# Kernel tuning notes

Measured on AMD Instinct MI355X. Metric: run time of the kernel, lower is better.

Reference implementation:

```python
import jax, jax.numpy as jnp
import numpy as np

N_NODES, IN_DIM, HID, LAT, N_EDGES = 50000, 3000, 512, 30, 800000
NEG_SLOPE = 0.2


def setup_inputs() -> dict:
    key = jax.random.key(0)
    ks = jax.random.split(key, 6)
    x = jax.random.normal(ks[0], (N_NODES, IN_DIM), dtype=jnp.float32)
    edge_index = jax.random.randint(ks[1], (2, N_EDGES), 0, N_NODES, dtype=jnp.int64)
    # xavier-normal-ish scales
    W1 = jax.random.normal(ks[2], (IN_DIM, HID), dtype=jnp.float32) * 0.02
    W2 = jax.random.normal(ks[3], (HID, LAT), dtype=jnp.float32) * 0.06
    att_src = jax.random.normal(ks[4], (HID,), dtype=jnp.float32) * 0.1
    att_dst = jax.random.normal(ks[5], (HID,), dtype=jnp.float32) * 0.1
    return {"x": x, "edge_index": edge_index, "W1": W1, "W2": W2,
            "att_src": att_src, "att_dst": att_dst}


def _segment_softmax(e, seg, num_segments):
    # numerically stable softmax over variable-degree dst neighborhoods
    m = jax.ops.segment_max(e, seg, num_segments=num_segments)
    m = jnp.where(jnp.isfinite(m), m, 0.0)  # empty segments -> 0, harmless
    p = jnp.exp(e - m[seg])
    s = jax.ops.segment_sum(p, seg, num_segments=num_segments)
    return p / (s[seg] + 1e-16)


def reference(x, edge_index, W1, W2, att_src, att_dst):
    N = x.shape[0]
    src, dst = edge_index[0], edge_index[1]  # messages flow src(j) -> dst(i)

    # ---- conv1: full GAT layer (heads=1, no self-loops, no bias) ----
    h1 = x @ W1                                   # [N, 512]
    a_src = h1 @ att_src                          # [N]
    a_dst = h1 @ att_dst                          # [N]
    e = jax.nn.leaky_relu(a_src[src] + a_dst[dst], NEG_SLOPE)  # [E]
    alpha = _segment_softmax(e, dst, N)           # [E] (also tied attn for conv3)
    agg1 = jax.ops.segment_sum(h1[src] * alpha[:, None], dst, num_segments=N)
    x1 = jax.nn.elu(agg1)                         # [N, 512]

    # ---- conv2: attention=False -> plain linear projection ----
    x2 = x1 @ W2                                  # [N, 30] (latent embedding)

    # ---- conv3: tied weights (W2^T) + tied attention from conv1 ----
    h3 = x2 @ W2.T                                # [N, 512]
    agg3 = jax.ops.segment_sum(h3[src] * alpha[:, None], dst, num_segments=N)
    x3 = jax.nn.elu(agg3)

    # ---- conv4: attention=False, tied weights (W1^T) ----
    x4 = x3 @ W1.T                                # [N, in_channels]
    return (x2, x4)
```

## Files before the change

### kernel.cpp

```cpp
#include <hip/hip_runtime.h>

#define N_NODES 50000
#define IN_DIM  3000
#define HID     512
#define LAT     30
#define N_EDGES 800000
#define M_PAD   50048
#define M_PAD2  50176
#define K1_PAD  3008
#define N4_PAD  3072

typedef __bf16 bf16;
typedef unsigned int uint;
typedef __attribute__((ext_vector_type(4))) float f32x4;
typedef __attribute__((ext_vector_type(8))) bf16 bf16x8;

__device__ __forceinline__ float bf2f(bf16 b){ return (float)b; }

__device__ __forceinline__ void gl16(const void* g, void* l){
  __builtin_amdgcn_global_load_lds(
      (const __attribute__((address_space(1))) void*)g,
      (__attribute__((address_space(3))) void*)l, 16, 0, 0);
}

__device__ __forceinline__ int xcd_swz(int orig, int nwg){
  int q = nwg >> 3, r = nwg & 7;
  int xcd = orig & 7, lid = orig >> 3;
  return (xcd < r ? xcd*(q+1) : r*(q+1) + (xcd-r)*q) + lid;
}

__global__ void k_w1t(const float* __restrict__ W1, bf16* __restrict__ W1T){
  int k = blockIdx.x*256 + threadIdx.x;
  int n = blockIdx.y;
  if (k >= K1_PAD) return;
  float v = (k < IN_DIM) ? W1[(long)k*HID + n] : 0.f;
  int kt = k >> 6, c = (k >> 3) & 7, off = k & 7;
  int p = c ^ (n & 7);
  W1T[(long)n*K1_PAD + kt*64 + p*8 + off] = (bf16)v;
}
__global__ void k_w1p(const float* __restrict__ W1, bf16* __restrict__ W1P){
  int k = blockIdx.x*256 + threadIdx.x;
  int n = blockIdx.y;
  if (k >= HID) return;
  float v = (n < IN_DIM) ? W1[(long)n*HID + k] : 0.f;
  int kt = k >> 6, c = (k >> 3) & 7, off = k & 7;
  int p = c ^ (n & 7);
  W1P[(long)n*HID + kt*64 + p*8 + off] = (bf16)v;
}
__global__ void k_w2t(const float* __restrict__ W2, bf16* __restrict__ W2T){
  int k = blockIdx.x*256 + threadIdx.x;
  int n = blockIdx.y;
  if (k >= HID) return;
  float v = (n < LAT) ? W2[(long)k*LAT + n] : 0.f;
  W2T[(long)n*HID + k] = (bf16)v;
}
__global__ void k_w2p(const float* __restrict__ W2, bf16* __restrict__ W2P){
  int t = blockIdx.x*256 + threadIdx.x;
  if (t >= HID*32) return;
  int n = t >> 5, k = t & 31;
  W2P[t] = (bf16)((k < LAT) ? W2[(long)n*LAT + k] : 0.f);
}

__global__ __launch_bounds__(256) void k_cvt(const float* __restrict__ x, bf16* __restrict__ xb){
  int chunk = blockIdx.x*256 + threadIdx.x;
  int row = blockIdx.y;
  if (chunk >= K1_PAD/8) return;
  int c8 = chunk*8;
  bf16x8 o;
  if (row < N_NODES && c8 + 8 <= IN_DIM){
    float4 v0 = *(const float4*)(x + (long)row*IN_DIM + c8);
    float4 v1 = *(const float4*)(x + (long)row*IN_DIM + c8 + 4);
    o[0]=(bf16)v0.x; o[1]=(bf16)v0.y; o[2]=(bf16)v0.z; o[3]=(bf16)v0.w;
    o[4]=(bf16)v1.x; o[5]=(bf16)v1.y; o[6]=(bf16)v1.z; o[7]=(bf16)v1.w;
  } else {
    #pragma unroll
    for (int j=0;j<8;j++){
      int c = c8 + j;
      float v = (row < N_NODES && c < IN_DIM) ? x[(long)row*IN_DIM + c] : 0.f;
      o[j] = (bf16)v;
    }
  }
  *(bf16x8*)(xb + (long)row*K1_PAD + c8) = o;
}

template<bool C_F32>
__global__ __launch_bounds__(512) void gemm8(
    const bf16* __restrict__ Agp, const bf16* __restrict__ Bgp, void* __restrict__ Cp,
    int lda, int ldb, int NT, int Mvalid, int Nvalid, int ldc, int NBX)
{
  __shared__ bf16 Af[2][256*64];
  __shared__ bf16 Bf[2][128*64];
  const int tid  = threadIdx.x;
  const int lane = tid & 63;
  const int w    = tid >> 6;
  const int wm   = (w >> 1) * 64;
  const int wn   = (w & 1) * 64;
  const int wgid = xcd_swz(blockIdx.x, gridDim.x);
  const int col0 = (wgid % NBX) * 128, row0 = (wgid / NBX) * 256;

  const int g   = lane >> 4;
  const int rl  = lane & 15;
  const int rx7 = rl & 7;

  f32x4 acc[4][4];
  #pragma unroll
  for (int mi=0;mi<4;mi++)
    #pragma unroll
    for (int ni=0;ni<4;ni++)
      acc[mi][ni] = (f32x4){0.f,0.f,0.f,0.f};

  bf16x8 a[4][2], B0[4][2], B1[4][2];

#define STAGE8(SLOT, T) do{                                                     \
    const long kb_ = (long)(T)*64;                                              \
    char* la_ = (char*)&Af[SLOT][0] + tid*16;                                   \
    _Pragma("unroll")                                                           \
    for (int i_=0;i_<4;i_++){                                                   \
      int row_ = i_*64 + (tid>>3);                                              \
      gl16(Agp + (long)(row0+row_)*lda + kb_ + (((tid&7)^(row_&7))<<3),         \
           la_ + i_*8192);                                                      \
    }                                                                           \
    char* lb_ = (char*)&Bf[SLOT][0] + tid*16;                                   \
    _Pragma("unroll")                                                           \
    for (int i_=0;i_<2;i_++){                                                   \
      int row_ = i_*64 + (tid>>3);                                              \
      gl16(Bgp + (long)(col0+row_)*ldb + kb_ + ((tid&7)<<3),                    \
           lb_ + i_*8192);                                                      \
    }                                                                           \
  }while(0)

#define RD_A(S, Q, KS) (*(const bf16x8*)((const char*)&Af[S][0] + \
    (wm + (Q)*16 + rl)*128 + ((((KS)*4 + g) ^ rx7)<<4)))
#define RD_B(S, NQ, KS) (*(const bf16x8*)((const char*)&Bf[S][0] + \
    (wn + (NQ)*16 + rl)*128 + ((((KS)*4 + g) ^ rx7)<<4)))

#define PHASE8(Q, BC, BN, SLOTN, DORD) do{                                      \
    __builtin_amdgcn_s_setprio(1);                                              \
    _Pragma("unroll")                                                           \
    for (int ni=0;ni<4;ni++)                                                    \
      acc[Q][ni] = __builtin_amdgcn_mfma_f32_16x16x32_bf16(a[Q][0], BC[ni][0], acc[Q][ni],0,0,0); \
    _Pragma("unroll")                                                           \
    for (int ni=0;ni<4;ni++)                                                    \
      acc[Q][ni] = __builtin_amdgcn_mfma_f32_16x16x32_bf16(a[Q][1], BC[ni][1], acc[Q][ni],0,0,0); \
    __builtin_amdgcn_s_setprio(0);                                              \
    if (DORD){                                                                  \
      a[Q][0]  = RD_A(SLOTN, Q, 0);  a[Q][1]  = RD_A(SLOTN, Q, 1);              \
      BN[Q][0] = RD_B(SLOTN, Q, 0);  BN[Q][1] = RD_B(SLOTN, Q, 1);              \
    }                                                                           \
  }while(0)

#define ITER8(T, SLOT, SLOTN, BC, BN) do{                                       \
    asm volatile("s_waitcnt vmcnt(0) lgkmcnt(0)" ::: "memory");                 \
    __builtin_amdgcn_s_barrier();                                               \
    __builtin_amdgcn_sched_barrier(0);                                          \
    if ((T)+2 < NT) STAGE8(SLOT, (T)+2);                                        \
    const bool dord_ = ((T)+1 < NT);                                            \
    PHASE8(0, BC, BN, SLOTN, dord_);                                            \
    PHASE8(1, BC, BN, SLOTN, dord_);                                            \
    PHASE8(2, BC, BN, SLOTN, dord_);                                            \
    PHASE8(3, BC, BN, SLOTN, dord_);                                            \
  }while(0)

  STAGE8(0, 0);
  asm volatile("s_waitcnt vmcnt(0)" ::: "memory");
  __builtin_amdgcn_s_barrier();
  if (NT > 1) STAGE8(1, 1);
  #pragma unroll
  for (int q=0;q<4;q++){
    a[q][0]  = RD_A(0, q, 0);  a[q][1]  = RD_A(0, q, 1);
    B0[q][0] = RD_B(0, q, 0);  B0[q][1] = RD_B(0, q, 1);
  }

  int t = 0;
  for (; t+1 < NT; t += 2){
    ITER8(t,   0, 1, B0, B1);
    ITER8(t+1, 1, 0, B1, B0);
  }
  if (t < NT) ITER8(t, 0, 1, B0, B1);

#undef ITER8
#undef PHASE8
#undef RD_A
#undef RD_B
#undef STAGE8

  const int crb  = (lane >> 4) * 4;
  const int ccol = lane & 15;
  #pragma unroll
  for (int mi=0;mi<4;mi++){
    #pragma unroll
    for (int v=0;v<4;v++){
      int r = row0 + wm + mi*16 + crb + v;
      if (r >= Mvalid) continue;
      #pragma unroll
      for (int ni=0;ni<4;ni++){
        int c = col0 + wn + ni*16 + ccol;
        if (c >= Nvalid) continue;
        float val = acc[mi][ni][v];
        if (C_F32) ((float*)Cp)[(long)r*ldc + c] = val;
        else       ((bf16*)Cp)[(long)r*ldc + c] = (bf16)val;
      }
    }
  }
}

template<bool C_F32, bool ELU>
__global__ __launch_bounds__(256) void gemm_glds(
    const bf16* __restrict__ A, const bf16* __restrict__ B, void* __restrict__ Cp,
    int lda, int ldb, int Ksteps, int Mvalid, int Nvalid, int ldc, int NBX)
{
  __shared__ bf16 Alds[2][128*32];
  __shared__ bf16 Blds[2][128*32];
  const int tid  = threadIdx.x;
  const int lane = tid & 63;
  const int w    = tid >> 6;
  const int wm   = (w >> 1) * 64, wn = (w & 1) * 64;
  const int wgid = xcd_swz(blockIdx.x, gridDim.x);
  const int col0 = (wgid % NBX) * 128, row0 = (wgid / NBX) * 128;

  f32x4 acc[4][4];
  #pragma unroll
  for (int mi=0;mi<4;mi++)
    #pragma unroll
    for (int ni=0;ni<4;ni++)
      acc[mi][ni] = (f32x4){0.f,0.f,0.f,0.f};

  const int sr = tid >> 2;
  const int sc = (tid & 3) * 16;
  const char* ga = (const char*)(A + (long)(row0 + sr) * lda) + sc;
  const char* gb = (const char*)(B + (long)(col0 + sr) * ldb) + sc;
  const long astep = (long)64 * lda * 2;
  const long bstep = (long)64 * ldb * 2;

#define STAGE_G(buf, ks) do{                                            \
    const long ko_ = (long)(ks) * 64;                                   \
    char* la_ = (char*)&Alds[buf][0] + sr*64 + sc;                      \
    char* lb_ = (char*)&Blds[buf][0] + sr*64 + sc;                      \
    gl16(ga + ko_,         la_);                                        \
    gl16(ga + ko_ + astep, la_ + 64*64);                                \
    gl16(gb + ko_,         lb_);                                        \
    gl16(gb + ko_ + bstep, lb_ + 64*64);                                \
  }while(0)

  STAGE_G(0, 0);

  for (int ks = 0; ks < Ksteps; ks++){
    const int cur = ks & 1;
    if (ks + 1 < Ksteps){
      STAGE_G(cur^1, ks+1);
      asm volatile("s_waitcnt vmcnt(4)" ::: "memory");
    } else {
      asm volatile("s_waitcnt vmcnt(0)" ::: "memory");
    }
    __builtin_amdgcn_s_barrier();

    const bf16* Ac = &Alds[cur][0];
    const bf16* Bc = &Blds[cur][0];
    bf16x8 af[4], bfr[4];
    #pragma unroll
    for (int mi=0;mi<4;mi++)
      af[mi] = *(const bf16x8*)&Ac[(wm + mi*16 + (lane & 15))*32 + (lane>>4)*8];
    #pragma unroll
    for (int ni=0;ni<4;ni++)
      bfr[ni] = *(const bf16x8*)&Bc[(wn + ni*16 + (lane & 15))*32 + (lane>>4)*8];
    #pragma unroll
    for (int mi=0;mi<4;mi++)
      #pragma unroll
      for (int ni=0;ni<4;ni++)
        acc[mi][ni] = __builtin_amdgcn_mfma_f32_16x16x32_bf16(af[mi], bfr[ni], acc[mi][ni], 0, 0, 0);

    __builtin_amdgcn_s_barrier();
  }
#undef STAGE_G

  const int crb  = (lane >> 4) * 4;
  const int ccol = lane & 15;
  #pragma unroll
  for (int mi=0;mi<4;mi++){
    #pragma unroll
    for (int v=0;v<4;v++){
      int r = row0 + wm + mi*16 + crb + v;
      if (r >= Mvalid) continue;
      #pragma unroll
      for (int ni=0;ni<4;ni++){
        int c = col0 + wn + ni*16 + ccol;
        if (c >= Nvalid) continue;
        float val = acc[mi][ni][v];
        if (ELU) val = (val > 0.f) ? val : expm1f(val);
        if (C_F32) ((float*)Cp)[(long)r*ldc + c] = val;
        else       ((bf16*)Cp)[(long)r*ldc + c] = (bf16)val;
      }
    }
  }
}

__global__ void k_attdots(const bf16* __restrict__ h1, const float* __restrict__ att_s,
                          const float* __restrict__ att_d, float* __restrict__ a_src,
                          float* __restrict__ a_dst){
  int gid = blockIdx.x * blockDim.x + threadIdx.x;
  int row = gid >> 6, lane = gid & 63;
  if (row >= N_NODES) return;
  bf16x8 hv = *(const bf16x8*)(h1 + (long)row*HID + lane*8);
  float s1 = 0.f, s2 = 0.f;
  #pragma unroll
  for (int j=0;j<8;j++){
    float h = bf2f(hv[j]);
    s1 = fmaf(h, att_s[lane*8+j], s1);
    s2 = fmaf(h, att_d[lane*8+j], s2);
  }
  #pragma unroll
  for (int o=32;o>0;o>>=1){ s1 += __shfl_down(s1,o); s2 += __shfl_down(s2,o); }
  if (lane == 0){ a_src[row] = s1; a_dst[row] = s2; }
}

__global__ void k_deg(const int* __restrict__ ei, int* __restrict__ deg){
  int e = blockIdx.x*256 + threadIdx.x;
  if (e >= N_EDGES) return;
  atomicAdd(&deg[ei[N_EDGES + e]], 1);
}

__global__ void k_scan(const int* __restrict__ deg, int* __restrict__ off, int* __restrict__ cur){
  const int n = M_PAD, T = 1024;
  int t = threadIdx.x;
  const int per = (n + T - 1) / T;
  int s0 = t*per, s1 = min(n, s0+per);
  int sum = 0;
  for (int i=s0;i<s1;i++) sum += deg[i];
  __shared__ int sd[1024];
  sd[t] = sum; __syncthreads();
  for (int o=1;o<T;o<<=1){
    int x = (t>=o) ? sd[t-o] : 0;
    __syncthreads();
    sd[t] += x;
    __syncthreads();
  }
  int run = sd[t] - sum;
  for (int i=s0;i<s1;i++){
    off[i] = run; cur[i] = run;
    run += deg[i];
  }
  if (s0 < n && s1 == n) off[n] = run;
}

__global__ void k_fill(const int* __restrict__ ei, int* __restrict__ cur,
                       int* __restrict__ csr_src, const float* __restrict__ a_s,
                       const float* __restrict__ a_d, float* __restrict__ p_e){
  int e = blockIdx.x*256 + threadIdx.x;
  if (e >= N_EDGES) return;
  int s = ei[e];
  int d = ei[N_EDGES + e];
  int pos = atomicAdd(&cur[d], 1);
  csr_src[pos] = s;
  float v = a_s[s] + a_d[d];
  v = (v > 0.f) ? v : 0.2f*v;
  p_e[pos] = __expf(v);
}

__global__ __launch_bounds__(256) void k_agg1w(
    const int* __restrict__ off, const int* __restrict__ csr_src,
    const float* __restrict__ p_edge,
    const bf16* __restrict__ h1, bf16* __restrict__ x1,
    float* __restrict__ s_node)
{
  const int i = blockIdx.x*4 + (threadIdx.x >> 6);
  const int lane = threadIdx.x & 63;
  if (i >= N_NODES) return;
  const int start = off[i];
  const int deg = off[i+1] - start;

  float acc[8];
  #pragma unroll
  for (int j=0;j<8;j++) acc[j] = 0.f;
  float ssum = 0.f;

  for (int k=0;k<deg;k++){
    int s = csr_src[start+k];
    float pk = p_edge[start+k];
    ssum += pk;
    bf16x8 hv = *(const bf16x8*)(h1 + (long)s*HID + lane*8);
    #pragma unroll
    for (int j=0;j<8;j++) acc[j] = fmaf(pk, bf2f(hv[j]), acc[j]);
  }
  float inv = 1.f/(ssum + 1e-16f);
  bf16x8 o;
  #pragma unroll
  for (int j=0;j<8;j++){
    float v = acc[j]*inv;
    v = (v > 0.f) ? v : expm1f(v);
    o[j] = (bf16)v;
  }
  *(bf16x8*)(x1 + (long)i*HID + lane*8) = o;
  if (lane == 0) s_node[i] = ssum;
}

__global__ void k_agg3(const int* __restrict__ off, const int* __restrict__ csr_src,
                       const float* __restrict__ p_edge, const float* __restrict__ s_node,
                       const float* __restrict__ x2, bf16* __restrict__ aggb)
{
  int i = blockIdx.x*8 + (threadIdx.x >> 5);
  int lane = threadIdx.x & 31;
  if (i >= M_PAD2) return;
  float acc = 0.f;
  if (i < N_NODES){
    int s0 = off[i], d = off[i+1] - s0;
    for (int k=0;k<d;k++){
      int s = csr_src[s0+k];
      float pk = p_edge[s0+k];
      if (lane < LAT) acc = fmaf(pk, x2[(long)s*LAT + lane], acc);
    }
    acc *= 1.f/(s_node[i] + 1e-16f);
  }
  aggb[(long)i*32 + lane] = (bf16)((lane < LAT) ? acc : 0.f);
}

extern "C" void kernel_launch(void* const* d_in, const int* in_sizes, int n_in,
                              void* d_out, int out_size, void* d_ws, size_t ws_size,
                              hipStream_t stream)
{
  const float* x     = (const float*)d_in[0];
  const int*   ei    = (const int*)d_in[1];
  const float* W1    = (const float*)d_in[2];
  const float* W2    = (const float*)d_in[3];
  const float* att_s = (const float*)d_in[4];
  const float* att_d = (const float*)d_in[5];

  float* out_x2 = (float*)d_out;
  float* out_x4 = (float*)d_out + (long)N_NODES*LAT;

  bf16* xb = (bf16*)out_x4;
  bf16* h1 = xb + (long)M_PAD2*K1_PAD;
  bf16* x1 = h1 + (long)M_PAD*HID;

  char* w = (char*)d_ws;
  bf16* W1T = (bf16*)w;  w += (long)HID*K1_PAD*2;
  bf16* W1P = (bf16*)w;  w += (long)N4_PAD*HID*2;
  bf16* W2T = (bf16*)w;  w += (long)128*HID*2;
  bf16* W2P = (bf16*)w;  w += (long)HID*32*2;
  bf16* x3  = (bf16*)w;  w += (long)M_PAD2*HID*2;
  bf16* aggb= (bf16*)w;  w += (long)M_PAD2*32*2;
  int* deg  = (int*)w;   w += (long)M_PAD*4;
  int* offs = (int*)w;   w += (long)(M_PAD+64)*4;
  int* cur  = (int*)w;   w += (long)M_PAD*4;
  int* csr  = (int*)w;   w += (long)N_EDGES*4;
  float* p_e = (float*)w; w += (long)N_EDGES*4;
  float* s_n = (float*)w; w += (long)M_PAD*4;
  float* a_s = (float*)w; w += (long)M_PAD*4;
  float* a_d = (float*)w; w += (long)M_PAD*4;

  k_w1t<<<dim3((K1_PAD+255)/256, HID), 256, 0, stream>>>(W1, W1T);
  k_w1p<<<dim3((HID+255)/256, N4_PAD), 256, 0, stream>>>(W1, W1P);
  k_w2t<<<dim3(2, 128), 256, 0, stream>>>(W2, W2T);
  k_w2p<<<(HID*32+255)/256, 256, 0, stream>>>(W2, W2P);
  k_cvt<<<dim3((K1_PAD/8+255)/256, M_PAD2), 256, 0, stream>>>(x, xb);

  hipMemsetAsync(deg, 0, (size_t)M_PAD*4, stream);
  k_deg<<<(N_EDGES+255)/256, 256, 0, stream>>>(ei, deg);
  k_scan<<<1, 1024, 0, stream>>>(deg, offs, cur);

  gemm8<false><<<(HID/128)*(M_PAD2/256), 512, 0, stream>>>(
      xb, W1T, h1, K1_PAD, K1_PAD, K1_PAD/64, N_NODES, HID, HID, HID/128);

  k_attdots<<<(N_NODES*64)/256, 256, 0, stream>>>(h1, att_s, att_d, a_s, a_d);

  k_fill<<<(N_EDGES+255)/256, 256, 0, stream>>>(ei, cur, csr, a_s, a_d, p_e);

  k_agg1w<<<(N_NODES+3)/4, 256, 0, stream>>>(offs, csr, p_e, h1, x1, s_n);

  gemm_glds<true,false><<<1*(M_PAD/128), 256, 0, stream>>>(
      x1, W2T, out_x2, HID, HID, HID/32, N_NODES, LAT, LAT, 1);

  k_agg3<<<(M_PAD2+7)/8, 256, 0, stream>>>(offs, csr, p_e, s_n, out_x2, aggb);
  gemm_glds<false,true><<<(HID/128)*(M_PAD2/128), 256, 0, stream>>>(
      aggb, W2P, x3, 32, 32, 1, M_PAD2, HID, HID, HID/128);

  gemm8<true><<<(N4_PAD/128)*(M_PAD2/256), 512, 0, stream>>>(
      x3, W1P, out_x4, HID, HID, HID/64, N_NODES, IN_DIM, IN_DIM, N4_PAD/128);
}
```

Measured before the change: 1.213 ms.

## Replace 256x128 GEMM kernel with 256x256-tile, K32-step double-buffered GEMM

Replaces the gemm8 kernel, used for both large projections (x@W1 and x3@W1^T), with gemm2. gemm2 uses a 256x256 output tile per 512-thread block, 32-wide K steps double-buffered through LDS via global_load_lds, and a simpler loop: one load stage, then a batch of 32 MFMAs per wave. The weight pre-pack kernels switch to a matching 32-element K-tile XOR swizzle. The larger tile aims to improve operand reuse and cut global and LDS traffic per FLOP. In exchange, the 128-float accumulator per lane under launch_bounds(512,2) risks register pressure or spills, and there are now two barriers per shorter K step and no register-level prefetch.

```diff
diff --git a/kernel.cpp b/kernel.cpp
--- a/kernel.cpp
+++ b/kernel.cpp
@@ -34,18 +34,18 @@
   int n = blockIdx.y;
   if (k >= K1_PAD) return;
   float v = (k < IN_DIM) ? W1[(long)k*HID + n] : 0.f;
-  int kt = k >> 6, c = (k >> 3) & 7, off = k & 7;
-  int p = c ^ (n & 7);
-  W1T[(long)n*K1_PAD + kt*64 + p*8 + off] = (bf16)v;
+  int kt = k >> 5, c = (k >> 3) & 3, off = k & 7;
+  int p = c ^ ((n >> 1) & 3);
+  W1T[(long)n*K1_PAD + kt*32 + p*8 + off] = (bf16)v;
 }
 __global__ void k_w1p(const float* __restrict__ W1, bf16* __restrict__ W1P){
   int k = blockIdx.x*256 + threadIdx.x;
   int n = blockIdx.y;
   if (k >= HID) return;
   float v = (n < IN_DIM) ? W1[(long)n*HID + k] : 0.f;
-  int kt = k >> 6, c = (k >> 3) & 7, off = k & 7;
-  int p = c ^ (n & 7);
-  W1P[(long)n*HID + kt*64 + p*8 + off] = (bf16)v;
+  int kt = k >> 5, c = (k >> 3) & 3, off = k & 7;
+  int p = c ^ ((n >> 1) & 3);
+  W1P[(long)n*HID + kt*32 + p*8 + off] = (bf16)v;
 }
 __global__ void k_w2t(const float* __restrict__ W2, bf16* __restrict__ W2T){
   int k = blockIdx.x*256 + threadIdx.x;
@@ -84,110 +84,81 @@
 }
 
 template<bool C_F32>
-__global__ __launch_bounds__(512) void gemm8(
-    const bf16* __restrict__ Agp, const bf16* __restrict__ Bgp, void* __restrict__ Cp,
-    int lda, int ldb, int NT, int Mvalid, int Nvalid, int ldc, int NBX)
+__global__ __launch_bounds__(512, 2) void gemm2(
+    const bf16* __restrict__ A, const bf16* __restrict__ B, void* __restrict__ Cp,
+    int lda, int ldb, int KS, int Mvalid, int Nvalid, int ldc, int NBX)
 {
-  __shared__ bf16 Af[2][256*64];
-  __shared__ bf16 Bf[2][128*64];
+  __shared__ bf16 Alds[2][256*32];
+  __shared__ bf16 Blds[2][256*32];
   const int tid  = threadIdx.x;
   const int lane = tid & 63;
   const int w    = tid >> 6;
-  const int wm   = (w >> 1) * 64;
-  const int wn   = (w & 1) * 64;
+  const int wm   = (w >> 2) * 128;
+  const int wn   = (w & 3) * 64;
   const int wgid = xcd_swz(blockIdx.x, gridDim.x);
-  const int col0 = (wgid % NBX) * 128, row0 = (wgid / NBX) * 256;
-
-  const int g   = lane >> 4;
-  const int rl  = lane & 15;
-  const int rx7 = rl & 7;
-
-  f32x4 acc[4][4];
-  #pragma unroll
-  for (int mi=0;mi<4;mi++)
+  const int col0 = (wgid % NBX) * 256, row0 = (wgid / NBX) * 256;
+
+  f32x4 acc[8][4];
+  #pragma unroll
+  for (int mi=0;mi<8;mi++)
     #pragma unroll
     for (int ni=0;ni<4;ni++)
       acc[mi][ni] = (f32x4){0.f,0.f,0.f,0.f};
 
-  bf16x8 a[4][2], B0[4][2], B1[4][2];
-
-#define STAGE8(SLOT, T) do{                                                     \
-    const long kb_ = (long)(T)*64;                                              \
-    char* la_ = (char*)&Af[SLOT][0] + tid*16;                                   \
-    _Pragma("unroll")                                                           \
-    for (int i_=0;i_<4;i_++){                                                   \
-      int row_ = i_*64 + (tid>>3);                                              \
-      gl16(Agp + (long)(row0+row_)*lda + kb_ + (((tid&7)^(row_&7))<<3),         \
-           la_ + i_*8192);                                                      \
-    }                                                                           \
-    char* lb_ = (char*)&Bf[SLOT][0] + tid*16;                                   \
-    _Pragma("unroll")                                                           \
-    for (int i_=0;i_<2;i_++){                                                   \
-      int row_ = i_*64 + (tid>>3);                                              \
-      gl16(Bgp + (long)(col0+row_)*ldb + kb_ + ((tid&7)<<3),                    \
-           lb_ + i_*8192);                                                      \
-    }                                                                           \
+  const int srow = tid >> 2;
+  const int acl  = (((tid & 3) ^ ((tid >> 3) & 3))) * 8;
+  const long a0 = (long)(row0 +       srow) * lda;
+  const long a1 = (long)(row0 + 128 + srow) * lda;
+  const long b0 = (long)(col0 +       srow) * ldb + (tid & 3) * 8;
+  const long b1 = (long)(col0 + 128 + srow) * ldb + (tid & 3) * 8;
+
+#define STG2(buf, ks) do{                                               \
+    const int kb_ = (ks) * 32;                                          \
+    char* la_ = (char*)&Alds[buf][0] + tid*16;                          \
+    char* lb_ = (char*)&Blds[buf][0] + tid*16;                          \
+    gl16(A + a0 + kb_ + acl, la_);                                      \
+    gl16(A + a1 + kb_ + acl, la_ + 8192);                               \
+    gl16(B + b0 + kb_, lb_);                                            \
+    gl16(B + b1 + kb_, lb_ + 8192);                                     \
   }while(0)
 
-#define RD_A(S, Q, KS) (*(const bf16x8*)((const char*)&Af[S][0] + \
-    (wm + (Q)*16 + rl)*128 + ((((KS)*4 + g) ^ rx7)<<4)))
-#define RD_B(S, NQ, KS) (*(const bf16x8*)((const char*)&Bf[S][0] + \
-    (wn + (NQ)*16 + rl)*128 + ((((KS)*4 + g) ^ rx7)<<4)))
-
-#define PHASE8(Q, BC, BN, SLOTN, DORD) do{                                      \
-    __builtin_amdgcn_s_setprio(1);                                              \
-    _Pragma("unroll")                                                           \
-    for (int ni=0;ni<4;ni++)                                                    \
-      acc[Q][ni] = __builtin_amdgcn_mfma_f32_16x16x32_bf16(a[Q][0], BC[ni][0], acc[Q][ni],0,0,0); \
-    _Pragma("unroll")                                                           \
-    for (int ni=0;ni<4;ni++)                                                    \
-      acc[Q][ni] = __builtin_amdgcn_mfma_f32_16x16x32_bf16(a[Q][1], BC[ni][1], acc[Q][ni],0,0,0); \
-    __builtin_amdgcn_s_setprio(0);                                              \
-    if (DORD){                                                                  \
-      a[Q][0]  = RD_A(SLOTN, Q, 0);  a[Q][1]  = RD_A(SLOTN, Q, 1);              \
-      BN[Q][0] = RD_B(SLOTN, Q, 0);  BN[Q][1] = RD_B(SLOTN, Q, 1);              \
-    }                                                                           \
-  }while(0)
-
-#define ITER8(T, SLOT, SLOTN, BC, BN) do{                                       \
-    asm volatile("s_waitcnt vmcnt(0) lgkmcnt(0)" ::: "memory");                 \
-    __builtin_amdgcn_s_barrier();                                               \
-    __builtin_amdgcn_sched_barrier(0);                                          \
-    if ((T)+2 < NT) STAGE8(SLOT, (T)+2);                                        \
-    const bool dord_ = ((T)+1 < NT);                                            \
-    PHASE8(0, BC, BN, SLOTN, dord_);                                            \
-    PHASE8(1, BC, BN, SLOTN, dord_);                                            \
-    PHASE8(2, BC, BN, SLOTN, dord_);                                            \
-    PHASE8(3, BC, BN, SLOTN, dord_);                                            \
-  }while(0)
-
-  STAGE8(0, 0);
-  asm volatile("s_waitcnt vmcnt(0)" ::: "memory");
-  __builtin_amdgcn_s_barrier();
-  if (NT > 1) STAGE8(1, 1);
-  #pragma unroll
-  for (int q=0;q<4;q++){
-    a[q][0]  = RD_A(0, q, 0);  a[q][1]  = RD_A(0, q, 1);
-    B0[q][0] = RD_B(0, q, 0);  B0[q][1] = RD_B(0, q, 1);
-  }
-
-  int t = 0;
-  for (; t+1 < NT; t += 2){
-    ITER8(t,   0, 1, B0, B1);
-    ITER8(t+1, 1, 0, B1, B0);
-  }
-  if (t < NT) ITER8(t, 0, 1, B0, B1);
-
-#undef ITER8
-#undef PHASE8
-#undef RD_A
-#undef RD_B
-#undef STAGE8
+  STG2(0, 0);
+
+  const int rl = lane & 15;
+  const int g  = lane >> 4;
+  const int ph = (g ^ ((rl >> 1) & 3)) * 16;
+
+  for (int ks = 0; ks < KS; ks++){
+    const int cur = ks & 1;
+    if (ks + 1 < KS){
+      STG2(cur^1, ks+1);
+      asm volatile("s_waitcnt vmcnt(4)" ::: "memory");
+    } else {
+      asm volatile("s_waitcnt vmcnt(0)" ::: "memory");
+    }
+    __builtin_amdgcn_s_barrier();
+
+    const char* Ac = (const char*)&Alds[cur][0] + (wm + rl)*64 + ph;
+    const char* Bc = (const char*)&Blds[cur][0] + (wn + rl)*64 + ph;
+    bf16x8 afr[8], bfr[4];
+    #pragma unroll
+    for (int mi=0;mi<8;mi++) afr[mi] = *(const bf16x8*)(Ac + mi*1024);
+    #pragma unroll
+    for (int ni=0;ni<4;ni++) bfr[ni] = *(const bf16x8*)(Bc + ni*1024);
+    #pragma unroll
+    for (int mi=0;mi<8;mi++)
+      #pragma unroll
+      for (int ni=0;ni<4;ni++)
+        acc[mi][ni] = __builtin_amdgcn_mfma_f32_16x16x32_bf16(afr[mi], bfr[ni], acc[mi][ni], 0, 0, 0);
+
+    __builtin_amdgcn_s_barrier();
+  }
+#undef STG2
 
   const int crb  = (lane >> 4) * 4;
   const int ccol = lane & 15;
   #pragma unroll
-  for (int mi=0;mi<4;mi++){
+  for (int mi=0;mi<8;mi++){
     #pragma unroll
     for (int v=0;v<4;v++){
       int r = row0 + wm + mi*16 + crb + v;
@@ -457,8 +428,8 @@
   k_deg<<<(N_EDGES+255)/256, 256, 0, stream>>>(ei, deg);
   k_scan<<<1, 1024, 0, stream>>>(deg, offs, cur);
 
-  gemm8<false><<<(HID/128)*(M_PAD2/256), 512, 0, stream>>>(
-      xb, W1T, h1, K1_PAD, K1_PAD, K1_PAD/64, N_NODES, HID, HID, HID/128);
+  gemm2<false><<<(HID/256)*(M_PAD2/256), 512, 0, stream>>>(
+      xb, W1T, h1, K1_PAD, K1_PAD, K1_PAD/32, N_NODES, HID, HID, HID/256);
 
   k_attdots<<<(N_NODES*64)/256, 256, 0, stream>>>(h1, att_s, att_d, a_s, a_d);
 
@@ -473,6 +444,6 @@
   gemm_glds<false,true><<<(HID/128)*(M_PAD2/128), 256, 0, stream>>>(
       aggb, W2P, x3, 32, 32, 1, M_PAD2, HID, HID, HID/128);
 
-  gemm8<true><<<(N4_PAD/128)*(M_PAD2/256), 512, 0, stream>>>(
-      x3, W1P, out_x4, HID, HID, HID/64, N_NODES, IN_DIM, IN_DIM, N4_PAD/128);
-}
+  gemm2<true><<<(N4_PAD/256)*(M_PAD2/256), 512, 0, stream>>>(
+      x3, W1P, out_x4, HID, HID, HID/32, N_NODES, IN_DIM, IN_DIM, N4_PAD/256);
+}
```

Result: no change. 1.190 ms (-1.9%).
